# Performance work log

Measured on AMD Instinct MI355X. Metric: run time of the kernel, lower is better.

Reference implementation:

```python
import jax, jax.numpy as jnp
import numpy as np

N_NODES = 50000
N_EDGES = 800000
D_IN = 128
D_OUT = 128


def _gcn_conv(x, W, b, src, dst, num_nodes):
    """PyG GCNConv: h = x @ W^T; symmetric-normalized mean over neighbors
    (with self-loops); out = aggregate + bias.
    src/dst already include self-loops."""
    h = x @ W.T  # [N, C_out]
    ones = jnp.ones(dst.shape[0], dtype=x.dtype)
    deg = jax.ops.segment_sum(ones, dst, num_segments=num_nodes)  # in-degree incl self-loop
    deg_inv_sqrt = jnp.where(deg > 0, jax.lax.rsqrt(deg), 0.0)
    norm = deg_inv_sqrt[src] * deg_inv_sqrt[dst]  # [E+N]
    msgs = h[src] * norm[:, None]  # gather + scale
    out = jax.ops.segment_sum(msgs, dst, num_segments=num_nodes)  # scatter-add
    return out + b


def setup_inputs() -> dict:
    key = jax.random.key(0)
    ks = jax.random.split(key, 9)
    x_r1 = jax.random.normal(ks[0], (N_NODES, D_IN), dtype=jnp.float32)
    x_r2 = jax.random.normal(ks[1], (N_NODES, D_IN), dtype=jnp.float32)
    x_i1 = jax.random.normal(ks[2], (N_NODES, D_IN), dtype=jnp.float32)
    x_i2 = jax.random.normal(ks[3], (N_NODES, D_IN), dtype=jnp.float32)
    edge_index = jax.random.randint(ks[4], (2, N_EDGES), 0, N_NODES, dtype=jnp.int64)
    s = 1.0 / np.sqrt(D_IN)
    W1 = jax.random.uniform(ks[5], (D_OUT, D_IN), minval=-s, maxval=s, dtype=jnp.float32)
    W2 = jax.random.uniform(ks[6], (D_OUT, D_IN), minval=-s, maxval=s, dtype=jnp.float32)
    b1 = jax.random.uniform(ks[7], (D_OUT,), minval=-s, maxval=s, dtype=jnp.float32)
    b2 = jax.random.uniform(ks[8], (D_OUT,), minval=-s, maxval=s, dtype=jnp.float32)
    return {"x_r1": x_r1, "x_r2": x_r2, "x_i1": x_i1, "x_i2": x_i2,
            "edge_index": edge_index, "W1": W1, "b1": b1, "W2": W2, "b2": b2}


def reference(x_r1, x_r2, x_i1, x_i2, edge_index, W1, b1, W2, b2):
    num_nodes = x_r1.shape[0]
    loops = jnp.arange(num_nodes, dtype=edge_index.dtype)
    src = jnp.concatenate([edge_index[0], loops])  # add self-loops
    dst = jnp.concatenate([edge_index[1], loops])
    # real1/imag1 share (W1, b1); real2/imag2 share (W2, b2)
    h_r1 = _gcn_conv(x_r1, W1, b1, src, dst, num_nodes)
    h_r2 = _gcn_conv(x_r2, W2, b2, src, dst, num_nodes)
    h_i1 = _gcn_conv(x_i1, W1, b1, src, dst, num_nodes)
    h_i2 = _gcn_conv(x_i2, W2, b2, src, dst, num_nodes)
    return (h_r1, h_r2, h_i1, h_i2)
```

## Files before the change

### kernel.cpp

```cpp
#include <hip/hip_runtime.h>

#define DD 128

typedef __bf16 bf16x8 __attribute__((ext_vector_type(8)));
typedef float f32x4 __attribute__((ext_vector_type(4)));

static __device__ __forceinline__ unsigned short f2bf(float f) {
    unsigned int u = __float_as_uint(f);
    u += 0x7FFF + ((u >> 16) & 1);
    return (unsigned short)(u >> 16);
}


__global__ __launch_bounds__(1024) void k_front(
    const int* __restrict__ dst, int* __restrict__ cnt,
    const float* __restrict__ W1, const float* __restrict__ W2,
    unsigned short* __restrict__ wbf, int E)
{
    const int bid = blockIdx.x;
    if (bid < 8) {
        int i = bid * 1024 + threadIdx.x;
        float4 v = (i < 4096) ? ((const float4*)W1)[i] : ((const float4*)W2)[i - 4096];
        ushort4 b;
        b.x = f2bf(v.x); b.y = f2bf(v.y); b.z = f2bf(v.z); b.w = f2bf(v.w);
        *(ushort4*)&wbf[(size_t)i * 4] = b;
        return;
    }
    int e4 = ((bid - 8) * 1024 + threadIdx.x) * 4;
    if (e4 < E) {
        int4 d = *(const int4*)&dst[e4];
        atomicAdd(&cnt[d.x], 1); atomicAdd(&cnt[d.y], 1);
        atomicAdd(&cnt[d.z], 1); atomicAdd(&cnt[d.w], 1);
    }
}


__global__ __launch_bounds__(1024) void k_scan1(const int* __restrict__ cnt,
                                                int* __restrict__ rp,
                                                float* __restrict__ dinv,
                                                int* __restrict__ bsum, int N) {
    __shared__ int wsum[16];
    const int tid = threadIdx.x, lane = tid & 63, wid = tid >> 6;
    const int i = blockIdx.x * 1024 + tid;
    int v = (i < N) ? cnt[i] : 0;
    int s = v;
    for (int off = 1; off < 64; off <<= 1) {
        int t = __shfl_up(s, off, 64);
        if (lane >= off) s += t;
    }
    if (lane == 63) wsum[wid] = s;
    __syncthreads();
    int woff = 0, total = 0;
#pragma unroll
    for (int w2 = 0; w2 < 16; ++w2) {
        int t = wsum[w2];
        if (w2 < wid) woff += t;
        total += t;
    }
    if (i < N) {
        rp[i + 1] = woff + s;
        dinv[i] = rsqrtf((float)(v + 1));
    }
    if (tid == 0) bsum[blockIdx.x] = total;
}

__global__ __launch_bounds__(1024) void k_scan2(const int* __restrict__ bsum,
                                                int* __restrict__ rp, int N) {
    __shared__ int boff_s;
    const int tid = threadIdx.x;
    if (tid < 64) {
        int v = (tid < (int)blockIdx.x) ? bsum[tid] : 0;
        for (int off = 32; off > 0; off >>= 1) v += __shfl_down(v, off, 64);
        if (tid == 0) boff_s = v;
    }
    __syncthreads();
    const int i = blockIdx.x * 1024 + tid;
    if (i < N) rp[i + 1] += boff_s;
    if (i == 0) rp[0] = 0;
}


__global__ __launch_bounds__(512) void k_mid(
    const float* __restrict__ x0, const float* __restrict__ x1,
    const float* __restrict__ x2, const float* __restrict__ x3,
    const unsigned short* __restrict__ wbf,
    unsigned short* __restrict__ h,
    const int* __restrict__ ei, const int* __restrict__ rp,
    int* __restrict__ cnt, const float* __restrict__ dinv,
    int2* __restrict__ csr,
    int N, int E, int GB)
{
    const int bid = blockIdx.x;
    const int tid = threadIdx.x;

    if (bid >= GB) {
        int e2 = ((bid - GB) * 512 + tid) * 2;
        if (e2 >= E) return;
        int2 s = *(const int2*)&ei[e2];
        int2 d = *(const int2*)&ei[E + e2];
        int o0 = atomicSub(&cnt[d.x], 1);
        csr[rp[d.x] + o0 - 1] = make_int2(s.x, __float_as_int(dinv[s.x]));
        int o1 = atomicSub(&cnt[d.y], 1);
        csr[rp[d.y] + o1 - 1] = make_int2(s.y, __float_as_int(dinv[s.y]));
        return;
    }

    const int m = bid & 3;
    const float* x = (m == 0) ? x0 : (m == 1) ? x1 : (m == 2) ? x2 : x3;
    const unsigned short* Wg = wbf + (size_t)(m & 1) * 128 * 128;

    __shared__ unsigned short smem[128 * 136];

    const int n0   = (bid >> 2) * 128;
    const int w    = tid >> 6;
    const int lane = tid & 63;
    const int am   = lane & 15;
    const int aq   = lane >> 4;
    const int r0   = w * 16;

    int arow = n0 + r0 + am; if (arow > N - 1) arow = N - 1;
    const float* xr = x + (size_t)arow * DD + aq * 8;
    float4 a0[4], a1[4];
#pragma unroll
    for (int q = 0; q < 4; ++q) {
        a0[q] = *(const float4*)(xr + q * 32);
        a1[q] = *(const float4*)(xr + q * 32 + 4);
    }

#pragma unroll
    for (int t = tid; t < 2048; t += 512)
        ((uint4*)smem)[t ^ ((t >> 4) & 7)] = ((const uint4*)Wg)[t];
    __syncthreads();

    bf16x8 afr[4];
#pragma unroll
    for (int q = 0; q < 4; ++q) {
        afr[q][0] = (__bf16)a0[q].x; afr[q][1] = (__bf16)a0[q].y;
        afr[q][2] = (__bf16)a0[q].z; afr[q][3] = (__bf16)a0[q].w;
        afr[q][4] = (__bf16)a1[q].x; afr[q][5] = (__bf16)a1[q].y;
        afr[q][6] = (__bf16)a1[q].z; afr[q][7] = (__bf16)a1[q].w;
    }

    f32x4 acc[8] = {};
#pragma unroll
    for (int q = 0; q < 4; ++q) {
        const int kc = q * 32 + aq * 8;
#pragma unroll
        for (int ct = 0; ct < 8; ++ct) {
            bf16x8 bf = *(const bf16x8*)&smem[(ct * 16 + am) * 128 +
                                              (kc ^ ((am & 7) << 3))];
            acc[ct] = __builtin_amdgcn_mfma_f32_16x16x32_bf16(afr[q], bf, acc[ct], 0, 0, 0);
        }
    }
    __syncthreads();

    const int cc = lane & 15;
    const int rr = (lane >> 4) * 4;
#pragma unroll
    for (int ct = 0; ct < 8; ++ct)
#pragma unroll
        for (int i = 0; i < 4; ++i)
            smem[(r0 + rr + i) * 136 + ct * 16 + cc] = f2bf(acc[ct][i]);
    __syncthreads();

#pragma unroll
    for (int k = 0; k < 4; ++k) {
        int f = k * 512 + tid;
        int row2 = f >> 4, ch = f & 15;
        int n = n0 + row2;
        if (n < N)
            *(uint4*)(h + ((size_t)n * 4 + m) * DD + ch * 8) =
                *(const uint4*)&smem[row2 * 136 + ch * 8];
    }
}


static __device__ __forceinline__ void acc8(float* a, uint4 v, float wt) {
    a[0] += __uint_as_float(v.x << 16) * wt;
    a[1] += __uint_as_float(v.x & 0xffff0000u) * wt;
    a[2] += __uint_as_float(v.y << 16) * wt;
    a[3] += __uint_as_float(v.y & 0xffff0000u) * wt;
    a[4] += __uint_as_float(v.z << 16) * wt;
    a[5] += __uint_as_float(v.z & 0xffff0000u) * wt;
    a[6] += __uint_as_float(v.w << 16) * wt;
    a[7] += __uint_as_float(v.w & 0xffff0000u) * wt;
}

__global__ __launch_bounds__(256) void k_gather(
    const int* __restrict__ rp, const int2* __restrict__ csr,
    const float* __restrict__ dinv, const unsigned short* __restrict__ h,
    const float* __restrict__ b1, const float* __restrict__ b2,
    float* __restrict__ out, int N)
{
    const int n = blockIdx.x * 4 + (threadIdx.x >> 6);
    if (n >= N) return;
    const int lane = threadIdx.x & 63;
    const int m    = lane >> 4;
    const int c    = (lane & 15) * 8;
    const size_t off = (size_t)lane * 8;

    const float dn = dinv[n];
    float a[8];

    {
        const float sn = dn * dn;
        const float* bb = (m & 1) ? b2 : b1;
        uint4 hv = *(const uint4*)(h + (size_t)n * 512 + off);
        float4 bv0 = *(const float4*)(bb + c);
        float4 bv1 = *(const float4*)(bb + c + 4);
        a[0] = bv0.x; a[1] = bv0.y; a[2] = bv0.z; a[3] = bv0.w;
        a[4] = bv1.x; a[5] = bv1.y; a[6] = bv1.z; a[7] = bv1.w;
        acc8(a, hv, sn);
    }

    int jb = rp[n];
    const int j1 = rp[n + 1];

    for (; jb + 7 < j1; jb += 8) {
        int2 e0 = csr[jb],     e1 = csr[jb + 1], e2 = csr[jb + 2], e3 = csr[jb + 3];
        int2 e4 = csr[jb + 4], e5 = csr[jb + 5], e6 = csr[jb + 6], e7 = csr[jb + 7];
        float w0 = __int_as_float(e0.y) * dn, w1 = __int_as_float(e1.y) * dn,
              w2 = __int_as_float(e2.y) * dn, w3 = __int_as_float(e3.y) * dn,
              w4 = __int_as_float(e4.y) * dn, w5 = __int_as_float(e5.y) * dn,
              w6 = __int_as_float(e6.y) * dn, w7 = __int_as_float(e7.y) * dn;
        uint4 v0 = *(const uint4*)(h + (size_t)e0.x * 512 + off);
        uint4 v1 = *(const uint4*)(h + (size_t)e1.x * 512 + off);
        uint4 v2 = *(const uint4*)(h + (size_t)e2.x * 512 + off);
        uint4 v3 = *(const uint4*)(h + (size_t)e3.x * 512 + off);
        uint4 v4 = *(const uint4*)(h + (size_t)e4.x * 512 + off);
        uint4 v5 = *(const uint4*)(h + (size_t)e5.x * 512 + off);
        uint4 v6 = *(const uint4*)(h + (size_t)e6.x * 512 + off);
        uint4 v7 = *(const uint4*)(h + (size_t)e7.x * 512 + off);
        acc8(a, v0, w0); acc8(a, v1, w1); acc8(a, v2, w2); acc8(a, v3, w3);
        acc8(a, v4, w4); acc8(a, v5, w5); acc8(a, v6, w6); acc8(a, v7, w7);
    }
    if (jb < j1) {
        const int last = j1 - 1;
#pragma unroll
        for (int k = 0; k < 8; ++k) {
            int idx = jb + k;
            int2 e = csr[idx <= last ? idx : last];
            float wt = (idx <= last) ? __int_as_float(e.y) * dn : 0.f;
            uint4 v = *(const uint4*)(h + (size_t)e.x * 512 + off);
            acc8(a, v, wt);
        }
    }

    float* po = out + ((size_t)m * N + n) * DD + c;
    f32x4 r0, r1;
    r0.x = a[0]; r0.y = a[1]; r0.z = a[2]; r0.w = a[3];
    r1.x = a[4]; r1.y = a[5]; r1.z = a[6]; r1.w = a[7];
    __builtin_nontemporal_store(r0, (f32x4*)po);
    __builtin_nontemporal_store(r1, (f32x4*)(po + 4));
}


extern "C" void kernel_launch(void* const* d_in, const int* in_sizes, int n_in,
                              void* d_out, int out_size, void* d_ws, size_t ws_size,
                              hipStream_t stream) {
    const float* x0 = (const float*)d_in[0];
    const float* x1 = (const float*)d_in[1];
    const float* x2 = (const float*)d_in[2];
    const float* x3 = (const float*)d_in[3];
    const int*   ei = (const int*)d_in[4];
    const float* W1 = (const float*)d_in[5];
    const float* b1 = (const float*)d_in[6];
    const float* W2 = (const float*)d_in[7];
    const float* b2 = (const float*)d_in[8];
    float* out = (float*)d_out;

    const int N = in_sizes[0] / DD;
    const int E = in_sizes[4] / 2;

    int*   cnt  = (int*)d_ws;
    int*   rp   = cnt + 65536;
    float* dinv = (float*)(rp + 65536);
    int*   bsum = (int*)(dinv + 65536);
    unsigned short* wbf = (unsigned short*)(bsum + 256);
    int2*  csr  = (int2*)(wbf + 2 * 128 * 128);
    unsigned short* h = (unsigned short*)(csr + E);

    const int nscan = (N + 1023) / 1024;
    const int GB    = ((N + 127) / 128) * 4;
    const int FB    = (E / 2 + 511) / 512;

    hipMemsetAsync(cnt, 0, (size_t)N * sizeof(int), stream);
    k_front<<<8 + (E / 4 + 1023) / 1024, 1024, 0, stream>>>(ei + E, cnt, W1, W2, wbf, E);
    k_scan1<<<nscan, 1024, 0, stream>>>(cnt, rp, dinv, bsum, N);
    k_scan2<<<nscan, 1024, 0, stream>>>(bsum, rp, N);
    k_mid  <<<GB + FB, 512, 0, stream>>>(x0, x1, x2, x3, wbf, h,
                                         ei, rp, cnt, dinv, csr, N, E, GB);
    k_gather<<<(N + 3) / 4, 256, 0, stream>>>(rp, csr, dinv, h, b1, b2, out, N);
}
```

Baseline: 394.9 us.

## Replace global atomic degree count with LDS partitioned histograms

Degree counting no longer uses global atomics. Blocks build shared-memory histograms over a node partition and an edge slice, then write per-slice partial counts into the CSR buffer, which is free at that point. The scan sums the 16 slices and initialises the cursor array, which also removes the memset. The cost is that each edge slice is read four times (once per partition), plus extra partial-count traffic.

```diff
diff --git a/kernel.cpp b/kernel.cpp
--- a/kernel.cpp
+++ b/kernel.cpp
@@ -1,6 +1,9 @@
 #include <hip/hip_runtime.h>
 
 #define DD 128
+#define PARTS 4
+#define SLICES 16
+#define PBINS 12544
 
 typedef __bf16 bf16x8 __attribute__((ext_vector_type(8)));
 typedef float f32x4 __attribute__((ext_vector_type(4)));
@@ -12,37 +15,74 @@
 }
 
 
-__global__ __launch_bounds__(1024) void k_front(
-    const int* __restrict__ dst, int* __restrict__ cnt,
+__global__ __launch_bounds__(1024) void k_count(
+    const int* __restrict__ dst, int* __restrict__ partial,
     const float* __restrict__ W1, const float* __restrict__ W2,
-    unsigned short* __restrict__ wbf, int E)
+    unsigned short* __restrict__ wbf, int N, int E)
 {
     const int bid = blockIdx.x;
-    if (bid < 8) {
-        int i = bid * 1024 + threadIdx.x;
+    const int tid = threadIdx.x;
+    if (bid >= PARTS * SLICES) {
+        int i = (bid - PARTS * SLICES) * 1024 + tid;
         float4 v = (i < 4096) ? ((const float4*)W1)[i] : ((const float4*)W2)[i - 4096];
         ushort4 b;
         b.x = f2bf(v.x); b.y = f2bf(v.y); b.z = f2bf(v.z); b.w = f2bf(v.w);
         *(ushort4*)&wbf[(size_t)i * 4] = b;
         return;
     }
-    int e4 = ((bid - 8) * 1024 + threadIdx.x) * 4;
-    if (e4 < E) {
-        int4 d = *(const int4*)&dst[e4];
-        atomicAdd(&cnt[d.x], 1); atomicAdd(&cnt[d.y], 1);
-        atomicAdd(&cnt[d.z], 1); atomicAdd(&cnt[d.w], 1);
-    }
-}
-
-
-__global__ __launch_bounds__(1024) void k_scan1(const int* __restrict__ cnt,
+
+    __shared__ int hist[PBINS];
+    const int p     = bid & (PARTS - 1);
+    const int c     = bid / PARTS;
+    const int psize = (N + PARTS - 1) / PARTS;
+    const int lo    = p * psize;
+
+    for (int t = tid; t < psize; t += 1024) hist[t] = 0;
+    __syncthreads();
+
+    const int sl = (E + SLICES - 1) / SLICES;
+    const int e0 = c * sl;
+    const int e1 = (e0 + sl < E) ? e0 + sl : E;
+
+    int e = e0 + tid * 4;
+    for (; e + 3 < e1; e += 4096) {
+        int4 d = *(const int4*)&dst[e];
+        unsigned t0 = (unsigned)(d.x - lo), t1 = (unsigned)(d.y - lo);
+        unsigned t2 = (unsigned)(d.z - lo), t3 = (unsigned)(d.w - lo);
+        if (t0 < (unsigned)psize) atomicAdd(&hist[t0], 1);
+        if (t1 < (unsigned)psize) atomicAdd(&hist[t1], 1);
+        if (t2 < (unsigned)psize) atomicAdd(&hist[t2], 1);
+        if (t3 < (unsigned)psize) atomicAdd(&hist[t3], 1);
+    }
+    if (e < e1) {
+        for (int k = e; k < e1; ++k) {
+            unsigned t0 = (unsigned)(dst[k] - lo);
+            if (t0 < (unsigned)psize) atomicAdd(&hist[t0], 1);
+        }
+    }
+    __syncthreads();
+
+    int* op = partial + (size_t)c * N;
+    for (int t = tid; t < psize; t += 1024) {
+        int g = lo + t;
+        if (g < N) op[g] = hist[t];
+    }
+}
+
+
+__global__ __launch_bounds__(1024) void k_scan1(const int* __restrict__ partial,
                                                 int* __restrict__ rp,
                                                 float* __restrict__ dinv,
+                                                int* __restrict__ cur,
                                                 int* __restrict__ bsum, int N) {
     __shared__ int wsum[16];
     const int tid = threadIdx.x, lane = tid & 63, wid = tid >> 6;
     const int i = blockIdx.x * 1024 + tid;
-    int v = (i < N) ? cnt[i] : 0;
+    int v = 0;
+    if (i < N) {
+#pragma unroll
+        for (int c = 0; c < SLICES; ++c) v += partial[c * N + i];
+    }
     int s = v;
     for (int off = 1; off < 64; off <<= 1) {
         int t = __shfl_up(s, off, 64);
@@ -60,6 +100,7 @@
     if (i < N) {
         rp[i + 1] = woff + s;
         dinv[i] = rsqrtf((float)(v + 1));
+        cur[i] = v;
     }
     if (tid == 0) bsum[blockIdx.x] = total;
 }
@@ -86,7 +127,7 @@
     const unsigned short* __restrict__ wbf,
     unsigned short* __restrict__ h,
     const int* __restrict__ ei, const int* __restrict__ rp,
-    int* __restrict__ cnt, const float* __restrict__ dinv,
+    int* __restrict__ cur, const float* __restrict__ dinv,
     int2* __restrict__ csr,
     int N, int E, int GB)
 {
@@ -98,9 +139,9 @@
         if (e2 >= E) return;
         int2 s = *(const int2*)&ei[e2];
         int2 d = *(const int2*)&ei[E + e2];
-        int o0 = atomicSub(&cnt[d.x], 1);
+        int o0 = atomicSub(&cur[d.x], 1);
         csr[rp[d.x] + o0 - 1] = make_int2(s.x, __float_as_int(dinv[s.x]));
-        int o1 = atomicSub(&cnt[d.y], 1);
+        int o1 = atomicSub(&cur[d.y], 1);
         csr[rp[d.y] + o1 - 1] = make_int2(s.y, __float_as_int(dinv[s.y]));
         return;
     }
@@ -272,23 +313,24 @@
     const int N = in_sizes[0] / DD;
     const int E = in_sizes[4] / 2;
 
-    int*   cnt  = (int*)d_ws;
-    int*   rp   = cnt + 65536;
+    int*   cur  = (int*)d_ws;
+    int*   rp   = cur + 65536;
     float* dinv = (float*)(rp + 65536);
     int*   bsum = (int*)(dinv + 65536);
     unsigned short* wbf = (unsigned short*)(bsum + 256);
     int2*  csr  = (int2*)(wbf + 2 * 128 * 128);
     unsigned short* h = (unsigned short*)(csr + E);
 
+    int* partial = (int*)csr;
+
     const int nscan = (N + 1023) / 1024;
     const int GB    = ((N + 127) / 128) * 4;
     const int FB    = (E / 2 + 511) / 512;
 
-    hipMemsetAsync(cnt, 0, (size_t)N * sizeof(int), stream);
-    k_front<<<8 + (E / 4 + 1023) / 1024, 1024, 0, stream>>>(ei + E, cnt, W1, W2, wbf, E);
-    k_scan1<<<nscan, 1024, 0, stream>>>(cnt, rp, dinv, bsum, N);
+    k_count<<<PARTS * SLICES + 8, 1024, 0, stream>>>(ei + E, partial, W1, W2, wbf, N, E);
+    k_scan1<<<nscan, 1024, 0, stream>>>(partial, rp, dinv, cur, bsum, N);
     k_scan2<<<nscan, 1024, 0, stream>>>(bsum, rp, N);
     k_mid  <<<GB + FB, 512, 0, stream>>>(x0, x1, x2, x3, wbf, h,
-                                         ei, rp, cnt, dinv, csr, N, E, GB);
+                                         ei, rp, cur, dinv, csr, N, E, GB);
     k_gather<<<(N + 3) / 4, 256, 0, stream>>>(rp, csr, dinv, h, b1, b2, out, N);
 }
```

Result: faster. 370.0 us (-6.3%).
